# Kernel optimization log

Hardware: AMD Instinct MI355X
Metric: run time of the kernel (lower is better)

The kernel has to match this reference:

```python
import jax, jax.numpy as jnp
import numpy as np

N, E, G = 50000, 400000, 2048
H, C = 4, 64            # heads, hidden per head
IN, ED, TASKS = 29, 6, 12
HC = H * C


def setup_inputs() -> dict:
    key = jax.random.key(0)
    ks = jax.random.split(key, 20)
    s = 0.1
    f32 = jnp.float32
    inp = {
        'x': jax.random.normal(ks[0], (N, IN), f32),
        'edge_index': jax.random.randint(ks[1], (2, E), 0, N),
        'edge_attr': jax.random.normal(ks[2], (E, ED), f32),
        'batch': jnp.sort(jax.random.randint(ks[3], (N,), 0, G)),
        # layer 1 (in=29 -> H*C=256)
        'W1': jax.random.normal(ks[4], (IN, HC), f32) * s,
        'as1': jax.random.normal(ks[5], (1, H, C), f32) * s,
        'ad1': jax.random.normal(ks[6], (1, H, C), f32) * s,
        'We1': jax.random.normal(ks[7], (ED, HC), f32) * s,
        'ae1': jax.random.normal(ks[8], (1, H, C), f32) * s,
        'b1': jnp.zeros((HC,), f32),
        # layer 2 (in=256 -> 256)
        'W2': jax.random.normal(ks[9], (HC, HC), f32) * s,
        'as2': jax.random.normal(ks[10], (1, H, C), f32) * s,
        'ad2': jax.random.normal(ks[11], (1, H, C), f32) * s,
        'We2': jax.random.normal(ks[12], (ED, HC), f32) * s,
        'ae2': jax.random.normal(ks[13], (1, H, C), f32) * s,
        'b2': jnp.zeros((HC,), f32),
        # readout linear (256 -> 12)
        'Wl': jax.random.normal(ks[14], (HC, TASKS), f32) * s,
        'bl': jnp.zeros((TASKS,), f32),
    }
    return inp


def _gat_conv(x, src, dst, eattr, W, a_src, a_dst, We, a_e, b):
    """PyG GATConv, concat=True, leaky_relu slope 0.2, self-loops already appended."""
    h = (x @ W).reshape(N, H, C)                      # [N,H,C]
    al_s = jnp.sum(h * a_src, axis=-1)                # [N,H]
    al_d = jnp.sum(h * a_dst, axis=-1)                # [N,H]
    he = (eattr @ We).reshape(-1, H, C)               # [Etot,H,C]
    al_e = jnp.sum(he * a_e, axis=-1)                 # [Etot,H]
    alpha = al_s[src] + al_d[dst] + al_e              # [Etot,H]
    alpha = jax.nn.leaky_relu(alpha, negative_slope=0.2)
    # segment softmax over incoming edges of each dst node
    amax = jax.ops.segment_max(alpha, dst, num_segments=N)
    ex = jnp.exp(alpha - amax[dst])
    denom = jax.ops.segment_sum(ex, dst, num_segments=N)
    alpha = ex / (denom[dst] + 1e-16)
    msg = h[src] * alpha[:, :, None]                  # [Etot,H,C]
    out = jax.ops.segment_sum(msg, dst, num_segments=N)
    return out.reshape(N, HC) + b


def reference(x, edge_index, edge_attr, batch,
              W1, as1, ad1, We1, ae1, b1,
              W2, as2, ad2, We2, ae2, b2, Wl, bl):
    # add self-loops with edge_attr fill = mean over existing edges (PyG default)
    loop = jnp.arange(N)
    src = jnp.concatenate([edge_index[0], loop])
    dst = jnp.concatenate([edge_index[1], loop])
    mean_e = jnp.mean(edge_attr, axis=0, keepdims=True)
    eattr = jnp.concatenate([edge_attr, jnp.broadcast_to(mean_e, (N, ED))], axis=0)

    h = _gat_conv(x, src, dst, eattr, W1, as1, ad1, We1, ae1, b1)
    h = jax.nn.relu(h)
    h = _gat_conv(h, src, dst, eattr, W2, as2, ad2, We2, ae2, b2)
    h = jax.nn.relu(h)

    # global mean pool over graphs
    sums = jax.ops.segment_sum(h, batch, num_segments=G)      # [G,HC]
    cnt = jax.ops.segment_sum(jnp.ones((N,), h.dtype), batch, num_segments=G)
    pooled = sums / jnp.maximum(cnt, 1.0)[:, None]
    return pooled @ Wl + bl
```

## Files before the change

kernel.cpp:

```cpp
#include <hip/hip_runtime.h>
#include <math.h>

static constexpr int NN = 50000;
static constexpr int EE = 400000;
static constexpr int GG = 2048;
static constexpr int TASKS = 12;

typedef __attribute__((ext_vector_type(8))) short short8;
typedef __attribute__((ext_vector_type(4))) float floatx4;

__device__ __forceinline__ unsigned short f2bf(float f) {
  unsigned u = __float_as_uint(f);
  u = u + 0x7fffu + ((u >> 16) & 1u);
  return (unsigned short)(u >> 16);
}
__device__ __forceinline__ float bflo(unsigned u) { return __uint_as_float(u << 16); }
__device__ __forceinline__ float bfhi(unsigned u) { return __uint_as_float(u & 0xffff0000u); }

static constexpr int NBDEG = (EE + 255) / 256;
static constexpr int NBMEAN = 256;
static constexpr int NBX = (NN * 4 + 255) / 256;
static constexpr int NW1 = 32;
static constexpr int NW2 = 256;
__global__ void k_pre(const int* __restrict__ dst, const float* __restrict__ ea,
                      const float* __restrict__ x, const float* __restrict__ W1,
                      const float* __restrict__ W2, int* __restrict__ deg,
                      float* __restrict__ msum, unsigned short* __restrict__ xb,
                      unsigned short* __restrict__ w1t, unsigned short* __restrict__ w2t) {
  const int b = blockIdx.x;
  const int t = threadIdx.x;
  if (b < NBDEG) {
    int e = b * 256 + t;
    if (e < EE) atomicAdd(&deg[dst[e]], 1);
  } else if (b < NBDEG + NBMEAN) {
    float s[6] = {0, 0, 0, 0, 0, 0};
    for (int e = (b - NBDEG) * 256 + t; e < EE; e += NBMEAN * 256) {
#pragma unroll
      for (int d = 0; d < 6; d++) s[d] += ea[(size_t)e * 6 + d];
    }
    __shared__ float ls[6];
    if (t < 6) ls[t] = 0.f;
    __syncthreads();
#pragma unroll
    for (int d = 0; d < 6; d++) atomicAdd(&ls[d], s[d]);
    __syncthreads();
    if (t < 6) atomicAdd(&msum[t], ls[t]);
  } else if (b < NBDEG + NBMEAN + NBX) {
    int i = (b - NBDEG - NBMEAN) * 256 + t;
    if (i < NN * 4) {
      int n = i >> 2, seg = i & 3;
      unsigned short v[8];
#pragma unroll
      for (int j = 0; j < 8; j++) {
        int k = seg * 8 + j;
        v[j] = (k < 29) ? f2bf(x[(size_t)n * 29 + k]) : (unsigned short)0;
      }
      *(short8*)(xb + (size_t)n * 32 + seg * 8) = *(short8*)v;
    }
  } else if (b < NBDEG + NBMEAN + NBX + NW1) {
    int i = (b - NBDEG - NBMEAN - NBX) * 256 + t;
    int row = i >> 5, k = i & 31;
    unsigned short v = (k < 29) ? f2bf(W1[(size_t)k * 256 + row]) : (unsigned short)0;
    w1t[((row >> 4) * 4 + (k >> 3)) * 128 + (row & 15) * 8 + (k & 7)] = v;
  } else {
    int i = (b - NBDEG - NBMEAN - NBX - NW1) * 256 + t;
    int row = i >> 8, k = i & 255;
    w2t[((row >> 4) * 32 + (k >> 3)) * 128 + (row & 15) * 8 + (k & 7)] = f2bf(W2[(size_t)k * 256 + row]);
  }
}

static constexpr int NBS = (NN + 255) / 256;

__global__ void k_scan1(const int* __restrict__ deg, int* __restrict__ rowptr,
                        int* __restrict__ bsums, const float* __restrict__ We1,
                        const float* __restrict__ ae1, const float* __restrict__ We2,
                        const float* __restrict__ ae2, const float* __restrict__ msum,
                        float* __restrict__ p1, float* __restrict__ p2) {
  const int t = threadIdx.x;
  if (blockIdx.x >= NBS) {
    const int layer = blockIdx.x - NBS;
    const float* We = layer ? We2 : We1;
    const float* ae = layer ? ae2 : ae1;
    float* params = layer ? p2 : p1;
    __shared__ float vsh[24];
    if (t < 24) {
      int d = t >> 2, h = t & 3;
      float s = 0.f;
      for (int c = 0; c < 64; c++) s += We[d * 256 + h * 64 + c] * ae[h * 64 + c];
      vsh[t] = s;
      params[t] = s;
    }
    __syncthreads();
    if (t < 4) {
      float s = 0.f;
      const float invE = 1.0f / (float)EE;
#pragma unroll
      for (int d = 0; d < 6; d++) s += (msum[d] * invE) * vsh[d * 4 + t];
      params[24 + t] = s;
    }
    return;
  }
  __shared__ int sh[256];
  int i = blockIdx.x * 256 + t;
  int v = (i < NN) ? deg[i] : 0;
  sh[t] = v;
  __syncthreads();
  for (int off = 1; off < 256; off <<= 1) {
    int tv = (t >= off) ? sh[t - off] : 0;
    __syncthreads();
    sh[t] += tv;
    __syncthreads();
  }
  if (i < NN) rowptr[i] = sh[t] - v;
  if (t == 255) bsums[blockIdx.x] = sh[255];
}

__global__ void k_scan23(int* __restrict__ rowptr, const int* __restrict__ bsums, int nb) {
  __shared__ int sh[256];
  const int t = threadIdx.x;
  sh[t] = (t < nb) ? bsums[t] : 0;
  __syncthreads();
  for (int off = 1; off < 256; off <<= 1) {
    int tv = (t >= off) ? sh[t - off] : 0;
    __syncthreads();
    sh[t] += tv;
    __syncthreads();
  }
  const int add = (blockIdx.x == 0) ? 0 : sh[blockIdx.x - 1];
  int i = blockIdx.x * 256 + t;
  if (i < NN) rowptr[i] += add;
  if (i == 0) rowptr[NN] = EE;
}

template <int KP>
__device__ __forceinline__ void gemm_body(
    int bx, const unsigned short* __restrict__ A, const unsigned short* __restrict__ Bt,
    const float* __restrict__ a_s, const float* __restrict__ a_d,
    unsigned short* __restrict__ Y, float* __restrict__ als, float* __restrict__ ald, int M) {
  __shared__ __align__(16) unsigned short Ash[64 * KP];
  const int tid = threadIdx.x;
  const int lane = tid & 63;
  const int w = tid >> 6;
  const int l15 = lane & 15;
  const int quad = lane >> 4;
  const int row0 = bx * 64;

  constexpr int STEPS = (64 * KP * 2) / (256 * 16);
  {
    const size_t limit = (size_t)M * (KP * 2) - 16;
    uint4 stg[STEPS];
#pragma unroll
    for (int s = 0; s < STEPS; s++) {
      size_t og = (size_t)row0 * (KP * 2) + s * 4096 + tid * 16;
      if (og > limit) og = limit;
      stg[s] = *(const uint4*)((const char*)A + og);
    }
#pragma unroll
    for (int s = 0; s < STEPS; s++) {
      int o = s * 4096 + tid * 16;
      int row = o / (KP * 2);
      *(uint4*)((char*)Ash + (o ^ ((row & 7) << 4))) = stg[s];
    }
  }

  floatx4 acc[4][4];
#pragma unroll
  for (int i = 0; i < 4; i++)
#pragma unroll
    for (int j = 0; j < 4; j++) acc[i][j] = {0.f, 0.f, 0.f, 0.f};

  const unsigned short* pb[4];
#pragma unroll
  for (int j = 0; j < 4; j++)
    pb[j] = Bt + (size_t)((w * 4 + j) * (KP / 8) + quad) * 128 + l15 * 8;

  constexpr int NPH = KP / 32;
  short8 bfr[3][4];
#pragma unroll
  for (int j = 0; j < 4; j++) bfr[0][j] = *(const short8*)pb[j];
  if (NPH > 1) {
#pragma unroll
    for (int j = 0; j < 4; j++) {
      pb[j] += 512;
      bfr[1][j] = *(const short8*)pb[j];
    }
  }

  __syncthreads();

  auto ldA = [&](int ph, short8 (&dst)[4]) {
#pragma unroll
    for (int i = 0; i < 4; i++) {
      int lin = (i * 16 + l15) * (KP * 2) + ph * 64 + quad * 16;
      dst[i] = *(const short8*)((const char*)Ash + (lin ^ ((l15 & 7) << 4)));
    }
  };
  short8 af[2][4];
  ldA(0, af[0]);

#pragma unroll
  for (int ph = 0; ph < NPH; ph++) {
    if (ph + 2 < NPH) {
#pragma unroll
      for (int j = 0; j < 4; j++) {
        pb[j] += 512;
        bfr[(ph + 2) % 3][j] = *(const short8*)pb[j];
      }
    }
    if (ph + 1 < NPH) ldA(ph + 1, af[(ph + 1) & 1]);
#pragma unroll
    for (int i = 0; i < 4; i++)
#pragma unroll
      for (int j = 0; j < 4; j++)
        acc[i][j] = __builtin_amdgcn_mfma_f32_16x16x32_bf16(af[ph & 1][i], bfr[ph % 3][j], acc[i][j], 0, 0, 0);
  }
  float asc[4], adc[4];
#pragma unroll
  for (int j = 0; j < 4; j++) {
    asc[j] = a_s[w * 64 + j * 16 + l15];
    adc[j] = a_d[w * 64 + j * 16 + l15];
  }
#pragma unroll
  for (int i = 0; i < 4; i++) {
#pragma unroll
    for (int r = 0; r < 4; r++) {
      const int row = row0 + i * 16 + quad * 4 + r;
      unsigned ub[4];
      float hv[4];
#pragma unroll
      for (int j = 0; j < 4; j++) {
        ub[j] = f2bf(acc[i][j][r]);
        hv[j] = __uint_as_float(ub[j] << 16);
      }
      if (row < M) {
#pragma unroll
        for (int j = 0; j < 4; j++) Y[(size_t)row * 256 + w * 64 + j * 16 + l15] = (unsigned short)ub[j];
      }
      float ps = hv[0] * asc[0] + hv[1] * asc[1] + hv[2] * asc[2] + hv[3] * asc[3];
      float pd = hv[0] * adc[0] + hv[1] * adc[1] + hv[2] * adc[2] + hv[3] * adc[3];
#pragma unroll
      for (int off = 1; off < 16; off <<= 1) {
        ps += __shfl_xor(ps, off, 64);
        pd += __shfl_xor(pd, off, 64);
      }
      if (l15 == 0 && row < M) {
        als[row * 4 + w] = ps;
        ald[row * 4 + w] = pd;
      }
    }
  }
}

static constexpr int GB = (NN + 63) / 64;

__global__ __launch_bounds__(256, 2) void k_scatgemm1(
    const int* __restrict__ ei, const int* __restrict__ rowptr, int* __restrict__ cursor,
    float* __restrict__ rec, const float* __restrict__ ea,
    const float* __restrict__ p1, const float* __restrict__ p2,
    const unsigned short* __restrict__ xb, const unsigned short* __restrict__ w1t,
    const float* __restrict__ as1, const float* __restrict__ ad1,
    unsigned short* __restrict__ hb, float* __restrict__ als, float* __restrict__ ald) {
  const int b = blockIdx.x;
  const int t = threadIdx.x;
  if (b < NBDEG) {
    int e = b * 256 + t;
    if (e >= EE) return;
    int s = ei[e];
    int d = ei[EE + e];
    int p = atomicAdd(&cursor[d], 1);
    int slot = rowptr[d] + p;
    const float* ep = ea + (size_t)e * 6;
    float2 e0 = *(const float2*)ep;
    float2 e1 = *(const float2*)(ep + 2);
    float2 e2 = *(const float2*)(ep + 4);
    float c1[4], c2[4];
#pragma unroll
    for (int h = 0; h < 4; h++) {
      c1[h] = e0.x * p1[0 * 4 + h] + e0.y * p1[1 * 4 + h] + e1.x * p1[2 * 4 + h] +
              e1.y * p1[3 * 4 + h] + e2.x * p1[4 * 4 + h] + e2.y * p1[5 * 4 + h];
      c2[h] = e0.x * p2[0 * 4 + h] + e0.y * p2[1 * 4 + h] + e1.x * p2[2 * 4 + h] +
              e1.y * p2[3 * 4 + h] + e2.x * p2[4 * 4 + h] + e2.y * p2[5 * 4 + h];
    }
    float* rp = rec + (size_t)slot * 16;
    *(float4*)rp = make_float4(__int_as_float(s), __int_as_float(e), 0.f, 0.f);
    *(float4*)(rp + 4) = make_float4(c1[0], c1[1], c1[2], c1[3]);
    *(float4*)(rp + 8) = make_float4(c2[0], c2[1], c2[2], c2[3]);
    *(float4*)(rp + 12) = make_float4(0.f, 0.f, 0.f, 0.f);
  } else {
    gemm_body<32>(b - NBDEG, xb, w1t, as1, ad1, hb, als, ald, NN);
  }
}

__global__ __launch_bounds__(256, 2) void k_gemm2(
    const unsigned short* __restrict__ A, const unsigned short* __restrict__ Bt,
    const float* __restrict__ a_s, const float* __restrict__ a_d,
    unsigned short* __restrict__ Y, float* __restrict__ als, float* __restrict__ ald) {
  gemm_body<256>(blockIdx.x, A, Bt, a_s, a_d, Y, als, ald, NN);
}

__device__ __forceinline__ float leaky02(float x) { return x > 0.f ? x : 0.2f * x; }

__global__ __launch_bounds__(256) void k_agg(
    const unsigned short* __restrict__ hinb, const float* __restrict__ als,
    const float* __restrict__ ald, const int* __restrict__ rowptr, const float* __restrict__ rec,
    int edoff, const float* __restrict__ params, const float* __restrict__ bias,
    unsigned short* __restrict__ houtb) {
  const int lane = threadIdx.x & 63;
  const int n = blockIdx.x * 4 + (threadIdx.x >> 6);
  if (n >= NN) return;
  const int half = lane >> 5;
  const int sl = lane & 31;
  const int head = sl >> 3;

  const float aldn = ald[n * 4 + head];
  float acc[8];
  float ssum;
  {
    float slg = leaky02(als[n * 4 + head] + aldn + params[24 + head]);
    float exs = __expf(slg);
    float wgt = (half == 0) ? exs : 0.f;
    ssum = wgt;
    uint4 uv = *(const uint4*)(hinb + (size_t)n * 256 + sl * 8);
    acc[0] = bflo(uv.x) * wgt;
    acc[1] = bfhi(uv.x) * wgt;
    acc[2] = bflo(uv.y) * wgt;
    acc[3] = bfhi(uv.y) * wgt;
    acc[4] = bflo(uv.z) * wgt;
    acc[5] = bfhi(uv.z) * wgt;
    acc[6] = bflo(uv.w) * wgt;
    acc[7] = bfhi(uv.w) * wgt;
  }
  const int end = rowptr[n + 1];
  int s = rowptr[n] + half;
  while (s < end) {
    int sid[4];
    float edv[4];
#pragma unroll
    for (int k = 0; k < 4; k++) {
      const int q = s + 2 * k;
      const bool v = q < end;
      const int idx = v ? q : end - 1;
      const float* rp = rec + (size_t)idx * 16;
      sid[k] = __float_as_int(rp[0]);
      edv[k] = v ? rp[edoff + head] : 0.f;
    }
    float alv[4];
#pragma unroll
    for (int k = 0; k < 4; k++) alv[k] = als[(size_t)sid[k] * 4 + head];
    uint4 r[4];
#pragma unroll
    for (int k = 0; k < 4; k++) {
      r[k] = make_uint4(0u, 0u, 0u, 0u);
      if (s + 2 * k < end) r[k] = *(const uint4*)(hinb + (size_t)sid[k] * 256 + sl * 8);
    }
#pragma unroll
    for (int k = 0; k < 4; k++) {
      const float ex = (s + 2 * k < end) ? __expf(leaky02(alv[k] + aldn + edv[k])) : 0.f;
      acc[0] += bflo(r[k].x) * ex;
      acc[1] += bfhi(r[k].x) * ex;
      acc[2] += bflo(r[k].y) * ex;
      acc[3] += bfhi(r[k].y) * ex;
      acc[4] += bflo(r[k].z) * ex;
      acc[5] += bfhi(r[k].z) * ex;
      acc[6] += bflo(r[k].w) * ex;
      acc[7] += bfhi(r[k].w) * ex;
      ssum += ex;
    }
    s += 8;
  }
#pragma unroll
  for (int j = 0; j < 8; j++) acc[j] += __shfl_xor(acc[j], 32, 64);
  ssum += __shfl_xor(ssum, 32, 64);
  if (half == 0) {
    const float inv = 1.f / (ssum + 1e-16f);
    float4 b0 = *(const float4*)(bias + sl * 8);
    float4 b1 = *(const float4*)(bias + sl * 8 + 4);
    const float bb[8] = {b0.x, b0.y, b0.z, b0.w, b1.x, b1.y, b1.z, b1.w};
    uint p[4];
#pragma unroll
    for (int j = 0; j < 4; j++) {
      float e0 = fmaxf(acc[2 * j] * inv + bb[2 * j], 0.f);
      float e1 = fmaxf(acc[2 * j + 1] * inv + bb[2 * j + 1], 0.f);
      p[j] = (uint)f2bf(e0) | ((uint)f2bf(e1) << 16);
    }
    *(uint4*)(houtb + (size_t)n * 256 + sl * 8) = make_uint4(p[0], p[1], p[2], p[3]);
  }
}

__global__ __launch_bounds__(256) void k_pool(const unsigned short* __restrict__ hb,
                                              const int* __restrict__ batch,
                                              const float* __restrict__ Wl,
                                              const float* __restrict__ bl,
                                              float* __restrict__ out) {
  int g = blockIdx.x;
  int t = threadIdx.x;
  int lo = 0, hi = NN;
  while (lo < hi) {
    int mid = (lo + hi) >> 1;
    if (batch[mid] < g) lo = mid + 1; else hi = mid;
  }
  int start = lo;
  hi = NN;
  while (lo < hi) {
    int mid = (lo + hi) >> 1;
    if (batch[mid] < g + 1) lo = mid + 1; else hi = mid;
  }
  int end = lo;
  const int mid2 = start + ((end - start) >> 1);
  __shared__ float sp[256], sq[256];
  {
    const int c = t & 127;
    const int hseg = t >> 7;
    const int a = hseg ? mid2 : start;
    const int b = hseg ? end : mid2;
    float s0 = 0.f, s1 = 0.f;
    for (int n2 = a; n2 < b; n2++) {
      uint u = ((const uint*)(hb + (size_t)n2 * 256))[c];
      s0 += bflo(u);
      s1 += bfhi(u);
    }
    float* dst = hseg ? sq : sp;
    dst[2 * c] = s0;
    dst[2 * c + 1] = s1;
  }
  __syncthreads();
  if (t < TASKS) {
    float invc = 1.f / fmaxf((float)(end - start), 1.f);
    float o = bl[t];
    for (int c = 0; c < 256; c++) o += (sp[c] + sq[c]) * invc * Wl[c * 12 + t];
    out[(size_t)g * 12 + t] = o;
  }
}

extern "C" void kernel_launch(void* const* d_in, const int* in_sizes, int n_in,
                              void* d_out, int out_size, void* d_ws, size_t ws_size,
                              hipStream_t stream) {
  const float* x = (const float*)d_in[0];
  const int* ei = (const int*)d_in[1];
  const float* ea = (const float*)d_in[2];
  const int* batch = (const int*)d_in[3];
  const float* W1 = (const float*)d_in[4];
  const float* as1 = (const float*)d_in[5];
  const float* ad1 = (const float*)d_in[6];
  const float* We1 = (const float*)d_in[7];
  const float* ae1 = (const float*)d_in[8];
  const float* b1 = (const float*)d_in[9];
  const float* W2 = (const float*)d_in[10];
  const float* as2 = (const float*)d_in[11];
  const float* ad2 = (const float*)d_in[12];
  const float* We2 = (const float*)d_in[13];
  const float* ae2 = (const float*)d_in[14];
  const float* b2 = (const float*)d_in[15];
  const float* Wl = (const float*)d_in[16];
  const float* bl = (const float*)d_in[17];
  float* out = (float*)d_out;

  char* ws = (char*)d_ws;
  size_t off = 0;
  auto take = [&](size_t bytes) -> char* {
    char* p = ws + off;
    off = (off + bytes + 255) & ~(size_t)255;
    return p;
  };
  float* msum = (float*)take(8 * 4);
  int* deg = (int*)take((size_t)NN * 4);
  int* cursor = (int*)take((size_t)NN * 4);
  size_t zero_end = off;
  int* rowptr = (int*)take((size_t)(NN + 1) * 4);
  int* bsums = (int*)take(256 * 4);
  float* rec = (float*)take((size_t)EE * 64);
  float* p1 = (float*)take(32 * 4);
  float* p2 = (float*)take(32 * 4);
  float* als = (float*)take((size_t)NN * 4 * 4);
  float* ald = (float*)take((size_t)NN * 4 * 4);
  unsigned short* hb = (unsigned short*)take((size_t)NN * 256 * 2);
  unsigned short* ab = (unsigned short*)take((size_t)NN * 256 * 2);
  unsigned short* xb = (unsigned short*)take((size_t)NN * 32 * 2);
  unsigned short* w1t = (unsigned short*)take((size_t)256 * 32 * 2);
  unsigned short* w2t = (unsigned short*)take((size_t)256 * 256 * 2);
  (void)ws_size;

  hipMemsetAsync(ws, 0, zero_end, stream);

  k_pre<<<NBDEG + NBMEAN + NBX + NW1 + NW2, 256, 0, stream>>>(ei + EE, ea, x, W1, W2,
                                                              deg, msum, xb, w1t, w2t);
  k_scan1<<<NBS + 2, 256, 0, stream>>>(deg, rowptr, bsums, We1, ae1, We2, ae2, msum, p1, p2);
  k_scan23<<<NBS, 256, 0, stream>>>(rowptr, bsums, NBS);

  k_scatgemm1<<<NBDEG + GB, 256, 0, stream>>>(ei, rowptr, cursor, rec, ea, p1, p2,
                                              xb, w1t, as1, ad1, hb, als, ald);

  k_agg<<<NN / 4, 256, 0, stream>>>(hb, als, ald, rowptr, rec, 4, p1, b1, ab);

  k_gemm2<<<GB, 256, 0, stream>>>(ab, w2t, as2, ad2, hb, als, ald);
  k_agg<<<NN / 4, 256, 0, stream>>>(hb, als, ald, rowptr, rec, 8, p2, b2, ab);

  k_pool<<<GG, 256, 0, stream>>>(ab, batch, Wl, bl, out);
}
```

Before: 286.2 us.

## Fuse mean-pool accumulation into second aggregation kernel via atomics

The second GAT aggregation kernel no longer writes the bf16 node features. Instead it stages each block's four node rows in shared memory, merges nodes that share a graph id, and atomically adds the sums into a zeroed fp32 pooled buffer. The old pool kernel, which re-read all node features, becomes a small readout that applies the mean and the linear layer. This removes a full write and re-read of the node features and keeps the pool sums in fp32, at the cost of more atomics and an extra block barrier. The early-return guard for out-of-range nodes is dropped, which is safe only because NN is a multiple of 4.

Result: no change. 284.2 us (-0.7%).

```diff
diff --git a/kernel.cpp b/kernel.cpp
--- a/kernel.cpp
+++ b/kernel.cpp
@@ -304,10 +304,13 @@
     const unsigned short* __restrict__ hinb, const float* __restrict__ als,
     const float* __restrict__ ald, const int* __restrict__ rowptr, const float* __restrict__ rec,
     int edoff, const float* __restrict__ params, const float* __restrict__ bias,
-    unsigned short* __restrict__ houtb) {
+    unsigned short* __restrict__ houtb, const int* __restrict__ batch,
+    float* __restrict__ pooled) {
+  __shared__ float lout[4][32][8];
+  __shared__ int lgs[4];
   const int lane = threadIdx.x & 63;
-  const int n = blockIdx.x * 4 + (threadIdx.x >> 6);
-  if (n >= NN) return;
+  const int wv = threadIdx.x >> 6;
+  const int n = blockIdx.x * 4 + wv;
   const int half = lane >> 5;
   const int sl = lane & 31;
   const int head = sl >> 3;
@@ -371,27 +374,51 @@
 #pragma unroll
   for (int j = 0; j < 8; j++) acc[j] += __shfl_xor(acc[j], 32, 64);
   ssum += __shfl_xor(ssum, 32, 64);
-  if (half == 0) {
-    const float inv = 1.f / (ssum + 1e-16f);
-    float4 b0 = *(const float4*)(bias + sl * 8);
-    float4 b1 = *(const float4*)(bias + sl * 8 + 4);
-    const float bb[8] = {b0.x, b0.y, b0.z, b0.w, b1.x, b1.y, b1.z, b1.w};
-    uint p[4];
-#pragma unroll
-    for (int j = 0; j < 4; j++) {
-      float e0 = fmaxf(acc[2 * j] * inv + bb[2 * j], 0.f);
-      float e1 = fmaxf(acc[2 * j + 1] * inv + bb[2 * j + 1], 0.f);
-      p[j] = (uint)f2bf(e0) | ((uint)f2bf(e1) << 16);
-    }
-    *(uint4*)(houtb + (size_t)n * 256 + sl * 8) = make_uint4(p[0], p[1], p[2], p[3]);
-  }
-}
-
-__global__ __launch_bounds__(256) void k_pool(const unsigned short* __restrict__ hb,
-                                              const int* __restrict__ batch,
-                                              const float* __restrict__ Wl,
-                                              const float* __restrict__ bl,
-                                              float* __restrict__ out) {
+
+  if (pooled == nullptr) {
+    if (half == 0) {
+      const float inv = 1.f / (ssum + 1e-16f);
+      float4 b0 = *(const float4*)(bias + sl * 8);
+      float4 b1 = *(const float4*)(bias + sl * 8 + 4);
+      const float bb[8] = {b0.x, b0.y, b0.z, b0.w, b1.x, b1.y, b1.z, b1.w};
+      uint p[4];
+#pragma unroll
+      for (int j = 0; j < 4; j++) {
+        float e0 = fmaxf(acc[2 * j] * inv + bb[2 * j], 0.f);
+        float e1 = fmaxf(acc[2 * j + 1] * inv + bb[2 * j + 1], 0.f);
+        p[j] = (uint)f2bf(e0) | ((uint)f2bf(e1) << 16);
+      }
+      *(uint4*)(houtb + (size_t)n * 256 + sl * 8) = make_uint4(p[0], p[1], p[2], p[3]);
+    }
+  } else {
+    if (lane == 0) lgs[wv] = batch[n];
+    if (half == 0) {
+      const float inv = 1.f / (ssum + 1e-16f);
+      float4 b0 = *(const float4*)(bias + sl * 8);
+      float4 b1 = *(const float4*)(bias + sl * 8 + 4);
+      const float bb[8] = {b0.x, b0.y, b0.z, b0.w, b1.x, b1.y, b1.z, b1.w};
+#pragma unroll
+      for (int j = 0; j < 8; j++) lout[wv][sl][j] = fmaxf(acc[j] * inv + bb[j], 0.f);
+    }
+    __syncthreads();
+    const int t = threadIdx.x;
+    int w0 = 0;
+    while (w0 < 4) {
+      const int gc = lgs[w0];
+      float sum = 0.f;
+      int w = w0;
+      for (; w < 4 && lgs[w] == gc; w++) sum += lout[w][t >> 3][t & 7];
+      atomicAdd(&pooled[(size_t)gc * 256 + t], sum);
+      w0 = w;
+    }
+  }
+}
+
+__global__ __launch_bounds__(64) void k_readout(const float* __restrict__ pooled,
+                                                const int* __restrict__ batch,
+                                                const float* __restrict__ Wl,
+                                                const float* __restrict__ bl,
+                                                float* __restrict__ out) {
   int g = blockIdx.x;
   int t = threadIdx.x;
   int lo = 0, hi = NN;
@@ -405,29 +432,12 @@
     int mid = (lo + hi) >> 1;
     if (batch[mid] < g + 1) lo = mid + 1; else hi = mid;
   }
-  int end = lo;
-  const int mid2 = start + ((end - start) >> 1);
-  __shared__ float sp[256], sq[256];
-  {
-    const int c = t & 127;
-    const int hseg = t >> 7;
-    const int a = hseg ? mid2 : start;
-    const int b = hseg ? end : mid2;
-    float s0 = 0.f, s1 = 0.f;
-    for (int n2 = a; n2 < b; n2++) {
-      uint u = ((const uint*)(hb + (size_t)n2 * 256))[c];
-      s0 += bflo(u);
-      s1 += bfhi(u);
-    }
-    float* dst = hseg ? sq : sp;
-    dst[2 * c] = s0;
-    dst[2 * c + 1] = s1;
-  }
-  __syncthreads();
+  int cnt = lo - start;
   if (t < TASKS) {
-    float invc = 1.f / fmaxf((float)(end - start), 1.f);
+    float invc = 1.f / fmaxf((float)cnt, 1.f);
     float o = bl[t];
-    for (int c = 0; c < 256; c++) o += (sp[c] + sq[c]) * invc * Wl[c * 12 + t];
+    const float* pg = pooled + (size_t)g * 256;
+    for (int c = 0; c < 256; c++) o += pg[c] * invc * Wl[c * 12 + t];
     out[(size_t)g * 12 + t] = o;
   }
 }
@@ -465,6 +475,7 @@
   float* msum = (float*)take(8 * 4);
   int* deg = (int*)take((size_t)NN * 4);
   int* cursor = (int*)take((size_t)NN * 4);
+  float* pooled = (float*)take((size_t)GG * 256 * 4);
   size_t zero_end = off;
   int* rowptr = (int*)take((size_t)(NN + 1) * 4);
   int* bsums = (int*)take(256 * 4);
@@ -490,10 +501,12 @@
   k_scatgemm1<<<NBDEG + GB, 256, 0, stream>>>(ei, rowptr, cursor, rec, ea, p1, p2,
                                               xb, w1t, as1, ad1, hb, als, ald);
 
-  k_agg<<<NN / 4, 256, 0, stream>>>(hb, als, ald, rowptr, rec, 4, p1, b1, ab);
+  k_agg<<<NN / 4, 256, 0, stream>>>(hb, als, ald, rowptr, rec, 4, p1, b1, ab,
+                                    batch, nullptr);
 
   k_gemm2<<<GB, 256, 0, stream>>>(ab, w2t, as2, ad2, hb, als, ald);
-  k_agg<<<NN / 4, 256, 0, stream>>>(hb, als, ald, rowptr, rec, 8, p2, b2, ab);
-
-  k_pool<<<GG, 256, 0, stream>>>(ab, batch, Wl, bl, out);
-}
+  k_agg<<<NN / 4, 256, 0, stream>>>(hb, als, ald, rowptr, rec, 8, p2, b2, ab,
+                                    batch, pooled);
+
+  k_readout<<<GG, 64, 0, stream>>>(pooled, batch, Wl, bl, out);
+}
```
